# Optimization experiments

Hardware: AMD Instinct MI355X
Metric: run time of the kernel (lower is better)

## Reference

```python
import jax, jax.numpy as jnp
import numpy as np

B, TU, TZ, V, H, E = 64, 128, 16, 32000, 512, 256
EPS = 1e-10


def setup_inputs() -> dict:
    key = jax.random.key(0)
    ks = jax.random.split(key, 22)
    s = 0.02  # weight init scale
    inp = {
        "embed_z": jax.random.normal(ks[0], (1, B, E), jnp.float32),
        "last_hidden": jax.random.normal(ks[1], (1, B, H), jnp.float32),
        "u_enc_out": jax.random.normal(ks[2], (TU, B, H), jnp.float32),
        # previous-turn z posterior: rows are probability distributions over vocab
        "pv_pz_proba": jax.nn.softmax(jax.random.normal(ks[3], (TZ, B, V), jnp.float32), axis=-1),
        "pv_z_dec_out": jax.random.normal(ks[4], (TZ, B, H), jnp.float32),
        "rand_eps": jax.random.normal(ks[5], (B, E), jnp.float32),
        "u_input_np": jax.random.randint(ks[6], (TU, B), 0, V),
        "u_input": jax.random.randint(ks[6], (TU, B), 0, V),   # unused by forward
        "m_input_np": jax.random.randint(ks[7], (TU, B), 0, V),  # unused by forward
        # GRU (single layer, single step)
        "W_ih": jax.random.normal(ks[8], (3 * H, E), jnp.float32) * s,
        "W_hh": jax.random.normal(ks[9], (3 * H, H), jnp.float32) * s,
        "b_ih": jnp.zeros((3 * H,), jnp.float32),
        "b_hh": jnp.zeros((3 * H,), jnp.float32),
        # w1: hidden -> vocab
        "W_w1": jax.random.normal(ks[10], (V, H), jnp.float32) * s,
        "b_w1": jnp.zeros((V,), jnp.float32),
        # proj_copy1 / proj_copy2: hidden -> hidden
        "W_p1": jax.random.normal(ks[11], (H, H), jnp.float32) * s,
        "b_p1": jnp.zeros((H,), jnp.float32),
        "W_p2": jax.random.normal(ks[12], (H, H), jnp.float32) * s,
        "b_p2": jnp.zeros((H,), jnp.float32),
        # mu / log_sigma: vocab -> embed
        "W_mu": jax.random.normal(ks[13], (E, V), jnp.float32) * s,
        "b_mu": jnp.zeros((E,), jnp.float32),
        "W_ls": jax.random.normal(ks[14], (E, V), jnp.float32) * s,
        "b_ls": jnp.zeros((E,), jnp.float32),
    }
    return inp


def reference(embed_z, last_hidden, u_enc_out, pv_pz_proba, pv_z_dec_out, rand_eps,
              u_input_np, u_input, m_input_np,
              W_ih, W_hh, b_ih, b_hh, W_w1, b_w1, W_p1, b_p1, W_p2, b_p2,
              W_mu, b_mu, W_ls, b_ls):
    # --- single GRU step (dropout is identity at rate 0 / eval) ---
    x = embed_z[0]          # (B,E)
    h0 = last_hidden[0]     # (B,H)
    gi = x @ W_ih.T + b_ih
    gh = h0 @ W_hh.T + b_hh
    i_r, i_z, i_n = jnp.split(gi, 3, axis=1)
    h_r, h_z, h_n = jnp.split(gh, 3, axis=1)
    r = jax.nn.sigmoid(i_r + h_r)
    z = jax.nn.sigmoid(i_z + h_z)
    n = jnp.tanh(i_n + r * h_n)
    h = (1.0 - z) * n + z * h0              # (B,H) == gru_out.squeeze(0)

    gen_score = h @ W_w1.T + b_w1           # (B,V)

    # --- user copy score (force_stable path): stable exp + scatter-add by token id ---
    uc = jnp.tanh(jnp.swapaxes(u_enc_out, 0, 1) @ W_p1.T + b_p1)   # (B,TU,H)
    us = jnp.einsum('bth,bh->bt', uc, h)                            # (B,TU)
    um = jnp.max(us, axis=1, keepdims=True)
    ue = jnp.exp(us - um)
    tok = u_input_np.T                                              # (B,TU)
    # sparse one-hot bmm == 1e-10 * sum_t e  +  scatter-add of e into vocab bin tok (tok!=0)
    scat = jnp.zeros((B, V), us.dtype).at[jnp.arange(B)[:, None], tok].add(
        ue * (tok != 0))
    u_copy = jnp.log(EPS * jnp.sum(ue, axis=1, keepdims=True) + scat) + um  # (B,V)

    # --- previous-z copy score (exp path taken when force_stable) ---
    # shift: drop last step, prepend 1e-10 fill
    shifted = jnp.concatenate(
        [jnp.full((1, B, V), EPS, pv_pz_proba.dtype), pv_pz_proba[:-1]], axis=0)  # (TZ,B,V)
    pc = jnp.tanh(jnp.swapaxes(pv_z_dec_out, 0, 1) @ W_p2.T + b_p2)  # (B,TZ,H)
    ps = jnp.exp(jnp.einsum('bth,bh->bt', pc, h))                    # (B,TZ)
    pv_copy = jnp.log(jnp.einsum('bt,tbv->bv', ps, shifted))         # (B,V)

    # --- joint softmax over [gen | u_copy | pv_copy], then merge ---
    scores = jax.nn.softmax(jnp.concatenate([gen_score, u_copy, pv_copy], axis=1), axis=1)
    g, u, p = jnp.split(scores, 3, axis=1)
    proba = g + u + p                        # (B,V)

    # --- VAE reparameterization ---
    appr_emb = proba @ W_mu.T + b_mu         # (B,E)
    log_sigma_ae = proba @ W_ls.T + b_ls
    sampled_ae = appr_emb + jnp.exp(log_sigma_ae) * rand_eps
    return sampled_ae, h[None], h[None], proba, appr_emb, log_sigma_ae
```

## Files before the change

### kernel.cpp

```cpp
#include <hip/hip_runtime.h>
#include <math.h>

#define B 64
#define TU 128
#define TZ 16
#define V 32000
#define H 512
#define E 256
#define EPSC 1e-10f
#define KMZ 125

typedef __attribute__((ext_vector_type(8))) short bf16x8;
typedef __attribute__((ext_vector_type(4))) float f32x4;
#define MFMA16(a, b, c) __builtin_amdgcn_mfma_f32_16x16x32_bf16((a), (b), (c), 0, 0, 0)

union U8 { uint4 u; bf16x8 b; };

__device__ __forceinline__ unsigned short f2bf(float f) {
  unsigned u = __float_as_uint(f);
  u += 0x7FFFu + ((u >> 16) & 1u);
  return (unsigned short)(u >> 16);
}
__device__ __forceinline__ unsigned pack2(float a, float b) {
  return (unsigned)f2bf(a) | ((unsigned)f2bf(b) << 16);
}

__device__ __forceinline__ void stage64x512(unsigned short* __restrict__ dst,
                                            const unsigned short* __restrict__ src)
{
  const int tid = threadIdx.x;
#pragma unroll
  for (int j = 0; j < 16; ++j) {
    const int f = j * 256 + tid;
    const int s = f * 8;
    const int row = s >> 9, col = s & 511;
    *(uint4*)&dst[row * 520 + col] = *(const uint4*)&src[s];
  }
}

__device__ __forceinline__ void stage64x512_f32(unsigned short* __restrict__ dst,
                                                const float* __restrict__ src)
{
  const int tid = threadIdx.x;
#pragma unroll
  for (int j = 0; j < 16; ++j) {
    const int f = j * 256 + tid;
    const int s = f * 8;
    const int row = s >> 9, col = s & 511;
    float4 a = *(const float4*)&src[s];
    float4 b = *(const float4*)&src[s + 4];
    uint4 o;
    o.x = pack2(a.x, a.y); o.y = pack2(a.z, a.w);
    o.z = pack2(b.x, b.y); o.w = pack2(b.z, b.w);
    *(uint4*)&dst[row * 520 + col] = o;
  }
}

__device__ void gemm64_body(const float* __restrict__ A, int lda,
                            const float* __restrict__ Bm, int ldb,
                            const float* __restrict__ bias,
                            float* __restrict__ C, int ldc,
                            int iters, int nb)
{
  __shared__ float As[64][33];
  __shared__ float Bs[64][33];
  const int tid = threadIdx.x;
  const int n0 = nb * 64;
  const int tv = tid & 15, tb = tid >> 4;
  const int lr = tid >> 3;
  const int lc = (tid & 7) << 2;
  float acc[4][4] = {};

  for (int it = 0; it < iters; ++it) {
    const int kb = it * 32;
    float4 a0 = *(const float4*)&A[(size_t)lr * lda + kb + lc];
    float4 a1 = *(const float4*)&A[(size_t)(lr + 32) * lda + kb + lc];
    float4 b0 = *(const float4*)&Bm[(size_t)(n0 + lr) * ldb + kb + lc];
    float4 b1 = *(const float4*)&Bm[(size_t)(n0 + lr + 32) * ldb + kb + lc];
    __syncthreads();
    As[lr][lc] = a0.x; As[lr][lc + 1] = a0.y; As[lr][lc + 2] = a0.z; As[lr][lc + 3] = a0.w;
    As[lr + 32][lc] = a1.x; As[lr + 32][lc + 1] = a1.y; As[lr + 32][lc + 2] = a1.z; As[lr + 32][lc + 3] = a1.w;
    Bs[lr][lc] = b0.x; Bs[lr][lc + 1] = b0.y; Bs[lr][lc + 2] = b0.z; Bs[lr][lc + 3] = b0.w;
    Bs[lr + 32][lc] = b1.x; Bs[lr + 32][lc + 1] = b1.y; Bs[lr + 32][lc + 2] = b1.z; Bs[lr + 32][lc + 3] = b1.w;
    __syncthreads();
#pragma unroll
    for (int kk = 0; kk < 32; ++kk) {
      float av[4], bv[4];
#pragma unroll
      for (int i = 0; i < 4; ++i) av[i] = As[tb * 4 + i][kk];
#pragma unroll
      for (int j = 0; j < 4; ++j) bv[j] = Bs[tv * 4 + j][kk];
#pragma unroll
      for (int i = 0; i < 4; ++i)
#pragma unroll
        for (int j = 0; j < 4; ++j) acc[i][j] += av[i] * bv[j];
    }
  }
#pragma unroll
  for (int i = 0; i < 4; ++i)
#pragma unroll
    for (int j = 0; j < 4; ++j) {
      const int n = n0 + tv * 4 + j;
      C[(size_t)(tb * 4 + i) * ldc + n] = acc[i][j] + bias[n];
    }
}

__global__ __launch_bounds__(256) void k1_prep(
    float* __restrict__ zbuf,
    const float* __restrict__ embed_z, const float* __restrict__ W_ih,
    const float* __restrict__ b_ih, float* __restrict__ gi,
    const float* __restrict__ last_hid, const float* __restrict__ W_hh,
    const float* __restrict__ b_hh, float* __restrict__ gh)
{
  const int bx = blockIdx.x;
  if (bx == 0) {
    for (int i = threadIdx.x; i < 42112; i += 256) zbuf[i] = 0.f;
  } else if (bx < 25) {
    gemm64_body(embed_z, E, W_ih, E, b_ih, gi, 1536, 8, bx - 1);
  } else {
    gemm64_body(last_hid, H, W_hh, H, b_hh, gh, 1536, 16, bx - 25);
  }
}

__global__ void gru_gates(const float* __restrict__ gi, const float* __restrict__ gh,
                          const float* __restrict__ h0, float* __restrict__ h,
                          float* __restrict__ oh1, float* __restrict__ oh2,
                          unsigned short* __restrict__ hbf)
{
  const int b = blockIdx.x, k = threadIdx.x;
  const float ir = gi[b * 1536 + k], iz = gi[b * 1536 + 512 + k], in_ = gi[b * 1536 + 1024 + k];
  const float hr = gh[b * 1536 + k], hz = gh[b * 1536 + 512 + k], hn = gh[b * 1536 + 1024 + k];
  const float r = 1.f / (1.f + __expf(-(ir + hr)));
  const float z = 1.f / (1.f + __expf(-(iz + hz)));
  const float n = tanhf(in_ + r * hn);
  const float hv = (1.f - z) * n + z * h0[b * H + k];
  h[b * H + k] = hv;
  oh1[b * H + k] = hv;
  oh2[b * H + k] = hv;
  hbf[b * H + k] = f2bf(hv);
}

__device__ void us_body_f32(unsigned short* __restrict__ Ws,
                            const float* __restrict__ A,
                            const float* __restrict__ Wm,
                            const float* __restrict__ bias,
                            const float* __restrict__ hvec,
                            float* __restrict__ outp, int T, int m0, int n0)
{
  stage64x512_f32(Ws, Wm + (size_t)n0 * 512);
  __syncthreads();

  const int tid = threadIdx.x;
  const int wave = tid >> 6, lane = tid & 63;
  const int l15 = lane & 15, l4 = lane >> 4;
  const int mbase = m0 + wave * 32;
  const float* ga = A + (size_t)(mbase + l15) * 512 + l4 * 8;

  f32x4 acc[2][4];
#pragma unroll
  for (int i = 0; i < 2; ++i)
#pragma unroll
    for (int j = 0; j < 4; ++j) acc[i][j] = (f32x4)0.f;

#pragma unroll
  for (int it = 0; it < 16; ++it) {
    bf16x8 af[2], bf[4];
#pragma unroll
    for (int i = 0; i < 2; ++i) {
      float4 a0 = *(const float4*)(ga + (size_t)i * 16 * 512 + it * 32);
      float4 a1 = *(const float4*)(ga + (size_t)i * 16 * 512 + it * 32 + 4);
      U8 u;
      u.u.x = pack2(a0.x, a0.y); u.u.y = pack2(a0.z, a0.w);
      u.u.z = pack2(a1.x, a1.y); u.u.w = pack2(a1.z, a1.w);
      af[i] = u.b;
    }
#pragma unroll
    for (int j = 0; j < 4; ++j)
      bf[j] = *(const bf16x8*)&Ws[(j * 16 + l15) * 520 + it * 32 + l4 * 8];
#pragma unroll
    for (int i = 0; i < 2; ++i)
#pragma unroll
      for (int j = 0; j < 4; ++j) acc[i][j] = MFMA16(af[i], bf[j], acc[i][j]);
  }

#pragma unroll
  for (int i = 0; i < 2; ++i) {
#pragma unroll
    for (int q = 0; q < 4; ++q) {
      const int r = mbase + i * 16 + l4 * 4 + q;
      const int b = r & 63;
      float sum = 0.f;
#pragma unroll
      for (int j = 0; j < 4; ++j) {
        const int col = n0 + j * 16 + l15;
        const float x = acc[i][j][q] + bias[col];
        const float ex = __expf(2.f * x);
        const float th = 1.f - 2.f / (ex + 1.f);
        sum += th * hvec[b * H + col];
      }
      sum += __shfl_xor(sum, 1);
      sum += __shfl_xor(sum, 2);
      sum += __shfl_xor(sum, 4);
      sum += __shfl_xor(sum, 8);
      if (l15 == 0) atomicAdd(&outp[b * T + (r >> 6)], sum);
    }
  }
}

__global__ __launch_bounds__(256) void k23(
    const unsigned short* __restrict__ h_bf, const float* __restrict__ W_w1,
    const float* __restrict__ b_w1, float* __restrict__ num,
    const float* __restrict__ u_enc, const float* __restrict__ W_p1,
    const float* __restrict__ b_p1,
    const float* __restrict__ pv_zdec, const float* __restrict__ W_p2,
    const float* __restrict__ b_p2,
    const float* __restrict__ h, float* __restrict__ us, float* __restrict__ pcs)
{
  __shared__ unsigned short sh[64 * 520];
  const int bx = blockIdx.x;
  const int tid = threadIdx.x;
  const int wave = tid >> 6, lane = tid & 63;
  const int l15 = lane & 15, l4 = lane >> 4;

  if (bx < 500) {
    const int n0 = bx * 64;
    const int nrow = n0 + (wave << 4) + l15;
    const float* gw = W_w1 + (size_t)nrow * 512 + l4 * 8;

    float4 wv[32];
#pragma unroll
    for (int it = 0; it < 16; ++it) {
      wv[2 * it]     = *(const float4*)(gw + it * 32);
      wv[2 * it + 1] = *(const float4*)(gw + it * 32 + 4);
    }

    stage64x512(sh, h_bf);
    __syncthreads();

    f32x4 acc[4];
#pragma unroll
    for (int i = 0; i < 4; ++i) acc[i] = (f32x4)0.f;

#pragma unroll
    for (int it = 0; it < 16; ++it) {
      U8 u;
      u.u.x = pack2(wv[2 * it].x, wv[2 * it].y);
      u.u.y = pack2(wv[2 * it].z, wv[2 * it].w);
      u.u.z = pack2(wv[2 * it + 1].x, wv[2 * it + 1].y);
      u.u.w = pack2(wv[2 * it + 1].z, wv[2 * it + 1].w);
#pragma unroll
      for (int i = 0; i < 4; ++i) {
        bf16x8 af = *(const bf16x8*)&sh[(i * 16 + l15) * 520 + it * 32 + l4 * 8];
        acc[i] = MFMA16(af, u.b, acc[i]);
      }
    }

    const float bv = b_w1[nrow];
#pragma unroll
    for (int i = 0; i < 4; ++i)
#pragma unroll
      for (int q = 0; q < 4; ++q) {
        const int row = i * 16 + l4 * 4 + q;
        num[(size_t)row * V + nrow] = acc[i][q] + bv;
      }
  } else if (bx < 1012) {
    const int idx = bx - 500;
    const int xcd = idx & 7, loc = idx >> 3;
    const int m0 = (xcd * 8 + (loc & 7)) * 128;
    const int n0 = (loc >> 3) * 64;
    us_body_f32(sh, u_enc, W_p1, b_p1, h, us, TU, m0, n0);
  } else {
    const int idx = bx - 1012;
    const int m0 = (idx & 7) * 128;
    const int n0 = (idx >> 3) * 64;
    us_body_f32(sh, pv_zdec, W_p2, b_p2, h, pcs, TZ, m0, n0);
  }
}

__global__ void smalls_kernel(const float* __restrict__ us, const float* __restrict__ pcs,
                              float* __restrict__ ue, float* __restrict__ base,
                              float* __restrict__ Kb)
{
  const int b = blockIdx.x, t = threadIdx.x;
  __shared__ float sm[128];
  __shared__ float sK;
  const float u = us[b * TU + t];
  sm[t] = u; __syncthreads();
  for (int s = 64; s > 0; s >>= 1) {
    if (t < s) sm[t] = fmaxf(sm[t], sm[t + s]);
    __syncthreads();
  }
  if (t == 0) {
    float um = sm[0];
    float pm = -1e30f;
    for (int q = 0; q < TZ; ++q) pm = fmaxf(pm, pcs[b * TZ + q]);
    sK = fmaxf(fmaxf(um, pm), 0.0f);
  }
  __syncthreads();
  const float K = sK;
  const float e = __expf(u - K);
  ue[b * TU + t] = e;
  sm[t] = e; __syncthreads();
  for (int s = 64; s > 0; s >>= 1) {
    if (t < s) sm[t] += sm[t + s];
    __syncthreads();
  }
  if (t == 0) {
    Kb[b] = K;
    base[b] = EPSC * sm[0] + EPSC * __expf(pcs[b * TZ + 0] - K);
  }
}

__global__ __launch_bounds__(256) void fuse3(
    float* __restrict__ num, const float* __restrict__ pv,
    const float* __restrict__ pcs, const float* __restrict__ ue,
    const float* __restrict__ base, const float* __restrict__ Kb,
    const int* __restrict__ tok, float* __restrict__ Z,
    unsigned short* __restrict__ nb)
{
  __shared__ float elds[2000];
  __shared__ float red[256];
  const int bx = blockIdx.x, tid = threadIdx.x;
  const int b = bx >> 4, c = bx & 15;
  const float K = Kb[b];
  const float bs = base[b];
  float w[15];
#pragma unroll
  for (int s = 0; s < 15; ++s) w[s] = __expf(pcs[b * TZ + s + 1] - K);
  float4* nrow = (float4*)&num[(size_t)b * V];
  ushort4* brow = (ushort4*)&nb[(size_t)b * V];
  const float4* pv4 = (const float4*)pv;
  const int f0 = c * 500;
#pragma unroll
  for (int ji = 0; ji < 2; ++ji) {
    const int i = tid + ji * 256;
    if (i < 500) {
      float4 g = nrow[f0 + i];
      float4 e;
      e.x = __expf(g.x - K) + bs;
      e.y = __expf(g.y - K) + bs;
      e.z = __expf(g.z - K) + bs;
      e.w = __expf(g.w - K) + bs;
#pragma unroll
      for (int s = 0; s < 15; ++s) {
        const float4 f = pv4[(size_t)(s * B + b) * (V / 4) + f0 + i];
        e.x += w[s] * f.x; e.y += w[s] * f.y;
        e.z += w[s] * f.z; e.w += w[s] * f.w;
      }
      ((float4*)elds)[i] = e;
    }
  }
  __syncthreads();
  if (tid < TU) {
    const int tk = tok[tid * B + b];
    if (tk != 0) {
      const int lo = c * 2000;
      if (tk >= lo && tk < lo + 2000) atomicAdd(&elds[tk - lo], ue[b * TU + tid]);
    }
  }
  __syncthreads();
  float loc = 0.f;
#pragma unroll
  for (int ji = 0; ji < 2; ++ji) {
    const int i = tid + ji * 256;
    if (i < 500) {
      float4 e = ((float4*)elds)[i];
      nrow[f0 + i] = e;
      ushort4 o;
      o.x = f2bf(e.x); o.y = f2bf(e.y); o.z = f2bf(e.z); o.w = f2bf(e.w);
      brow[f0 + i] = o;
      loc += e.x + e.y + e.z + e.w;
    }
  }
  red[tid] = loc; __syncthreads();
  for (int st = 128; st > 0; st >>= 1) {
    if (tid < st) red[tid] += red[tid + st];
    __syncthreads();
  }
  if (tid == 0) atomicAdd(&Z[b], red[0]);
}

__global__ __launch_bounds__(256) void norm2(float* __restrict__ num,
                                             const float* __restrict__ Z)
{
  const int b = blockIdx.y;
  const int i4 = blockIdx.x * 256 + threadIdx.x;
  if (i4 >= V / 4) return;
  const float r = 1.0f / Z[b];
  float4* row = (float4*)&num[(size_t)b * V];
  float4 v = row[i4];
  v.x *= r; v.y *= r; v.z *= r; v.w *= r;
  row[i4] = v;
}

__global__ __launch_bounds__(256) void k_muls(
    const unsigned short* __restrict__ Ab,
    const float* __restrict__ Wmu, const float* __restrict__ Wls,
    float* __restrict__ pmu, float* __restrict__ pls,
    int* __restrict__ cnt, const float* __restrict__ Z,
    const float* __restrict__ bmu, const float* __restrict__ bls,
    const float* __restrict__ eps_r, float* __restrict__ out)
{
  const int tid = threadIdx.x;
  const int wave = tid >> 6, lane = tid & 63;
  const int l15 = lane & 15, l4 = lane >> 4;
  const int cgx = blockIdx.x;
  const float* gW = blockIdx.y ? Wls : Wmu;
  float* pO = blockIdx.y ? pls : pmu;
  const int kb0 = blockIdx.z * 256;
  const int c0 = cgx * 128 + wave * 32;

  const unsigned short* ga = Ab + (size_t)l15 * V + kb0 + l4 * 8;
  const float* gw0 = gW + (size_t)(c0 + l15) * V + kb0 + l4 * 8;
  const float* gw1 = gW + (size_t)(c0 + 16 + l15) * V + kb0 + l4 * 8;

  f32x4 acc[4][2];
#pragma unroll
  for (int i = 0; i < 4; ++i)
#pragma unroll
    for (int j = 0; j < 2; ++j) acc[i][j] = (f32x4)0.f;

#pragma unroll
  for (int it = 0; it < 8; ++it) {
    const int o = it * 32;
    bf16x8 af[4];
#pragma unroll
    for (int i = 0; i < 4; ++i)
      af[i] = *(const bf16x8*)(ga + (size_t)i * 16 * V + o);
    float4 a0 = *(const float4*)(gw0 + o), a1 = *(const float4*)(gw0 + o + 4);
    float4 b0 = *(const float4*)(gw1 + o), b1 = *(const float4*)(gw1 + o + 4);
    U8 u0, u1;
    u0.u.x = pack2(a0.x, a0.y); u0.u.y = pack2(a0.z, a0.w);
    u0.u.z = pack2(a1.x, a1.y); u0.u.w = pack2(a1.z, a1.w);
    u1.u.x = pack2(b0.x, b0.y); u1.u.y = pack2(b0.z, b0.w);
    u1.u.z = pack2(b1.x, b1.y); u1.u.w = pack2(b1.z, b1.w);
#pragma unroll
    for (int i = 0; i < 4; ++i) {
      acc[i][0] = MFMA16(af[i], u0.b, acc[i][0]);
      acc[i][1] = MFMA16(af[i], u1.b, acc[i][1]);
    }
  }
#pragma unroll
  for (int i = 0; i < 4; ++i)
#pragma unroll
    for (int j = 0; j < 2; ++j) {
      const int col = c0 + j * 16 + l15;
#pragma unroll
      for (int q = 0; q < 4; ++q) {
        const int row = i * 16 + l4 * 4 + q;
        atomicAdd(&pO[row * E + col], acc[i][j][q]);
      }
    }

  __threadfence();
  __shared__ int lastf;
  if (tid == 0) lastf = (atomicAdd(cnt, 1) == 2 * 2 * KMZ - 1);
  __syncthreads();
  if (lastf) {
    __threadfence();
    const int e = tid;
    for (int b = 0; b < B; ++b) {
      const float rz = 1.0f / Z[b];
      const float ap = pmu[b * E + e] * rz + bmu[e];
      const float ls = pls[b * E + e] * rz + bls[e];
      out[b * E + e] = ap + __expf(ls) * eps_r[b * E + e];
      out[2129920 + b * E + e] = ap;
      out[2146304 + b * E + e] = ls;
    }
  }
}

extern "C" void kernel_launch(void* const* d_in, const int* in_sizes, int n_in,
                              void* d_out_v, int out_size, void* d_ws, size_t ws_size,
                              hipStream_t stream)
{
  (void)in_sizes; (void)n_in; (void)out_size; (void)ws_size;
  const float* embed_z    = (const float*)d_in[0];
  const float* last_hid   = (const float*)d_in[1];
  const float* u_enc      = (const float*)d_in[2];
  const float* pv_pz      = (const float*)d_in[3];
  const float* pv_zdec    = (const float*)d_in[4];
  const float* rand_eps   = (const float*)d_in[5];
  const int*   u_input_np = (const int*)d_in[6];
  const float* W_ih = (const float*)d_in[9];
  const float* W_hh = (const float*)d_in[10];
  const float* b_ih = (const float*)d_in[11];
  const float* b_hh = (const float*)d_in[12];
  const float* W_w1 = (const float*)d_in[13];
  const float* b_w1 = (const float*)d_in[14];
  const float* W_p1 = (const float*)d_in[15];
  const float* b_p1 = (const float*)d_in[16];
  const float* W_p2 = (const float*)d_in[17];
  const float* b_p2 = (const float*)d_in[18];
  const float* W_mu = (const float*)d_in[19];
  const float* b_mu = (const float*)d_in[20];
  const float* W_ls = (const float*)d_in[21];
  const float* b_ls = (const float*)d_in[22];
  float* d_out = (float*)d_out_v;

  float* ws   = (float*)d_ws;
  float* h    = ws;
  float* gi   = ws + 32768;
  float* gh   = ws + 131072;
  float* us   = ws + 229376;
  float* pcs  = ws + 237568;
  float* Z    = ws + 238592;
  float* pmu  = ws + 238656;
  float* pls  = ws + 255040;
  int*   cnt  = (int*)(ws + 271424);
  float* ue   = ws + 271488;
  float* base = ws + 279680;
  float* Kb   = ws + 279744;
  unsigned short* h_bf   = (unsigned short*)(ws + 279808);
  unsigned short* num_bf = (unsigned short*)(ws + 296192);

  float* num   = d_out + 81920;
  float* outh1 = d_out + 16384;
  float* outh2 = d_out + 49152;

  k1_prep<<<dim3(49), 256, 0, stream>>>(
      us ,
      embed_z, W_ih, b_ih, gi, last_hid, W_hh, b_hh, gh);

  gru_gates<<<dim3(B), 512, 0, stream>>>(gi, gh, last_hid, h, outh1, outh2, h_bf);

  k23<<<dim3(1076), 256, 0, stream>>>(
      h_bf, W_w1, b_w1, num,
      u_enc, W_p1, b_p1,
      pv_zdec, W_p2, b_p2,
      h, us, pcs);

  smalls_kernel<<<dim3(B), 128, 0, stream>>>(us, pcs, ue, base, Kb);

  fuse3<<<dim3(1024), 256, 0, stream>>>(num, pv_pz, pcs, ue, base, Kb,
                                        u_input_np, Z, num_bf);

  k_muls<<<dim3(2, 2, KMZ), 256, 0, stream>>>(
      num_bf, W_mu, W_ls, pmu, pls, cnt, Z, b_mu, b_ls, rand_eps, d_out);

  norm2<<<dim3(32, B), 256, 0, stream>>>(num, Z);
}
```

Baseline: 199.3 us.

## Split mu/log-sigma GEMM into more K-chunks with 4-way partial buffers and separate finalize

The K dimension of the mu/log-sigma projection is split into 250 chunks of 128 instead of 125 chunks of 256, which doubles the block count to fill more CUs. The chunks accumulate atomically into four separate partial buffers chosen by chunk index to spread atomic contention. The last-block-done counter epilogue is replaced by a separate final2 kernel that sums the partials and applies bias, exp and the noise term. Costs are an extra kernel launch, a larger zeroing pass in the prep kernel, and more total atomic traffic.

```diff
diff --git a/kernel.cpp b/kernel.cpp
--- a/kernel.cpp
+++ b/kernel.cpp
@@ -8,7 +8,6 @@
 #define H 512
 #define E 256
 #define EPSC 1e-10f
-#define KMZ 125
 
 typedef __attribute__((ext_vector_type(8))) short bf16x8;
 typedef __attribute__((ext_vector_type(4))) float f32x4;
@@ -114,7 +113,7 @@
 {
   const int bx = blockIdx.x;
   if (bx == 0) {
-    for (int i = threadIdx.x; i < 42112; i += 256) zbuf[i] = 0.f;
+    for (int i = threadIdx.x; i < 140352; i += 256) zbuf[i] = 0.f;
   } else if (bx < 25) {
     gemm64_body(embed_z, E, W_ih, E, b_ih, gi, 1536, 8, bx - 1);
   } else {
@@ -393,22 +392,18 @@
   row[i4] = v;
 }
 
-__global__ __launch_bounds__(256) void k_muls(
+__global__ __launch_bounds__(256, 2) void k_muls(
     const unsigned short* __restrict__ Ab,
     const float* __restrict__ Wmu, const float* __restrict__ Wls,
-    float* __restrict__ pmu, float* __restrict__ pls,
-    int* __restrict__ cnt, const float* __restrict__ Z,
-    const float* __restrict__ bmu, const float* __restrict__ bls,
-    const float* __restrict__ eps_r, float* __restrict__ out)
+    float* __restrict__ pmu, float* __restrict__ pls)
 {
   const int tid = threadIdx.x;
   const int wave = tid >> 6, lane = tid & 63;
   const int l15 = lane & 15, l4 = lane >> 4;
-  const int cgx = blockIdx.x;
   const float* gW = blockIdx.y ? Wls : Wmu;
-  float* pO = blockIdx.y ? pls : pmu;
-  const int kb0 = blockIdx.z * 256;
-  const int c0 = cgx * 128 + wave * 32;
+  float* pO = (blockIdx.y ? pls : pmu) + (blockIdx.z & 3) * (B * E);
+  const int kb0 = blockIdx.z * 128;
+  const int c0 = blockIdx.x * 128 + wave * 32;
 
   const unsigned short* ga = Ab + (size_t)l15 * V + kb0 + l4 * 8;
   const float* gw0 = gW + (size_t)(c0 + l15) * V + kb0 + l4 * 8;
@@ -421,7 +416,7 @@
     for (int j = 0; j < 2; ++j) acc[i][j] = (f32x4)0.f;
 
 #pragma unroll
-  for (int it = 0; it < 8; ++it) {
+  for (int it = 0; it < 4; ++it) {
     const int o = it * 32;
     bf16x8 af[4];
 #pragma unroll
@@ -451,23 +446,26 @@
         atomicAdd(&pO[row * E + col], acc[i][j][q]);
       }
     }
-
-  __threadfence();
-  __shared__ int lastf;
-  if (tid == 0) lastf = (atomicAdd(cnt, 1) == 2 * 2 * KMZ - 1);
-  __syncthreads();
-  if (lastf) {
-    __threadfence();
-    const int e = tid;
-    for (int b = 0; b < B; ++b) {
-      const float rz = 1.0f / Z[b];
-      const float ap = pmu[b * E + e] * rz + bmu[e];
-      const float ls = pls[b * E + e] * rz + bls[e];
-      out[b * E + e] = ap + __expf(ls) * eps_r[b * E + e];
-      out[2129920 + b * E + e] = ap;
-      out[2146304 + b * E + e] = ls;
-    }
-  }
+}
+
+__global__ void final2(const float* __restrict__ pmu, const float* __restrict__ pls,
+                       const float* __restrict__ Z,
+                       const float* __restrict__ bmu, const float* __restrict__ bls,
+                       const float* __restrict__ eps_r, float* __restrict__ out)
+{
+  const int b = blockIdx.x, e = threadIdx.x;
+  float smu = 0.f, sls = 0.f;
+#pragma unroll
+  for (int s = 0; s < 4; ++s) {
+    smu += pmu[s * (B * E) + b * E + e];
+    sls += pls[s * (B * E) + b * E + e];
+  }
+  const float rz = 1.0f / Z[b];
+  const float ap = smu * rz + bmu[e];
+  const float ls = sls * rz + bls[e];
+  out[b * E + e] = ap + __expf(ls) * eps_r[b * E + e];
+  out[2129920 + b * E + e] = ap;
+  out[2146304 + b * E + e] = ls;
 }
 
 extern "C" void kernel_launch(void* const* d_in, const int* in_sizes, int n_in,
@@ -506,13 +504,12 @@
   float* pcs  = ws + 237568;
   float* Z    = ws + 238592;
   float* pmu  = ws + 238656;
-  float* pls  = ws + 255040;
-  int*   cnt  = (int*)(ws + 271424);
-  float* ue   = ws + 271488;
-  float* base = ws + 279680;
-  float* Kb   = ws + 279744;
-  unsigned short* h_bf   = (unsigned short*)(ws + 279808);
-  unsigned short* num_bf = (unsigned short*)(ws + 296192);
+  float* pls  = ws + 304192;
+  float* ue   = ws + 369728;
+  float* base = ws + 377920;
+  float* Kb   = ws + 377984;
+  unsigned short* h_bf   = (unsigned short*)(ws + 378048);
+  unsigned short* num_bf = (unsigned short*)(ws + 394432);
 
   float* num   = d_out + 81920;
   float* outh1 = d_out + 16384;
@@ -535,8 +532,9 @@
   fuse3<<<dim3(1024), 256, 0, stream>>>(num, pv_pz, pcs, ue, base, Kb,
                                         u_input_np, Z, num_bf);
 
-  k_muls<<<dim3(2, 2, KMZ), 256, 0, stream>>>(
-      num_bf, W_mu, W_ls, pmu, pls, cnt, Z, b_mu, b_ls, rand_eps, d_out);
+  k_muls<<<dim3(2, 2, 250), 256, 0, stream>>>(num_bf, W_mu, W_ls, pmu, pls);
+
+  final2<<<dim3(B), 256, 0, stream>>>(pmu, pls, Z, b_mu, b_ls, rand_eps, d_out);
 
   norm2<<<dim3(32, B), 256, 0, stream>>>(num, Z);
 }
```

Result: faster. 170.3 us (-14.5%).
